# Performance work log

Measured on AMD Instinct MI355X. Metric: run time of the kernel, lower is better.

## Reference

```python
import jax, jax.numpy as jnp
import numpy as np

N_HEAD, D_MODEL, D_K, D_V, INPUT_DIM = 8, 512, 64, 64, 512
B, L = 16, 512
MASK_FILL = -1e32
LN_EPS = 1e-5


def layer_norm(x, g, b):
    m = jnp.mean(x, axis=-1, keepdims=True)
    var = jnp.mean(jnp.square(x - m), axis=-1, keepdims=True)
    return (x - m) * jax.lax.rsqrt(var + LN_EPS) * g + b


def setup_inputs() -> dict:
    key = jax.random.key(0)
    ks = jax.random.split(key, 9)
    std_qk = np.sqrt(2.0 / (D_MODEL + D_K)).astype(np.float32)
    std_v = np.sqrt(2.0 / (D_MODEL + D_V)).astype(np.float32)
    inp = {
        "q": jax.random.normal(ks[0], (B, L, INPUT_DIM), jnp.float32),
        "k": jax.random.normal(ks[1], (B, L, INPUT_DIM), jnp.float32),
        "v": jax.random.normal(ks[2], (B, L, INPUT_DIM), jnp.float32),
        # projection weights, torch Linear convention [out, in]
        "Wq": jax.random.normal(ks[3], (N_HEAD * D_K, INPUT_DIM), jnp.float32) * std_qk,
        "Wk": jax.random.normal(ks[4], (N_HEAD * D_K, INPUT_DIM), jnp.float32) * std_qk,
        "Wv": jax.random.normal(ks[5], (N_HEAD * D_V, INPUT_DIM), jnp.float32) * std_v,
        "fc1_w": jax.random.normal(ks[6], (D_MODEL, N_HEAD * D_V), jnp.float32) * 0.02,
        "fc2_w": jax.random.normal(ks[7], (D_MODEL, N_HEAD * D_V), jnp.float32) * 0.02,
        "ln1_g": jnp.ones((INPUT_DIM,), jnp.float32),
        "ln1_b": jnp.zeros((INPUT_DIM,), jnp.float32),
        "ln2_g": jnp.ones((INPUT_DIM,), jnp.float32),
        "ln2_b": jnp.zeros((INPUT_DIM,), jnp.float32),
        "ln3_g": jnp.ones((INPUT_DIM,), jnp.float32),
        "ln3_b": jnp.zeros((INPUT_DIM,), jnp.float32),
    }
    return inp


def reference(q, k, v, Wq, Wk, Wv, fc1_w, fc2_w,
              ln1_g, ln1_b, ln2_g, ln2_b, ln3_g, ln3_b):
    b, lq, _ = q.shape
    qn = layer_norm(q, ln1_g, ln1_b)
    kn = layer_norm(k, ln2_g, ln2_b)
    vn = layer_norm(v, ln3_g, ln3_b)
    # projections -> [B, L, H, d]
    qh = (qn @ Wq.T).reshape(b, lq, N_HEAD, D_K)
    kh = (kn @ Wk.T).reshape(b, lq, N_HEAD, D_K)
    vh = (vn @ Wv.T).reshape(b, lq, N_HEAD, D_V)
    # scaled dot-product attention with diagonal mask (diag_mask_flag=True)
    attn = jnp.einsum('bqhd,bkhd->bhqk', qh, kh) / jnp.sqrt(jnp.float32(D_K))
    eye = jnp.eye(lq, dtype=bool)  # diag entries masked out
    attn = jnp.where(eye[None, None], MASK_FILL, attn)
    attn = jax.nn.softmax(attn, axis=-1)
    dynamic = jnp.einsum('bhqk,bkhd->bqhd', attn, vh).reshape(b, lq, N_HEAD * D_V)
    static = vh.reshape(b, lq, N_HEAD * D_V)
    dynamic = dynamic @ fc1_w.T
    static = static @ fc2_w.T
    # attn returned in the torch layout [n_head*B, L, L] (head-major)
    attn_out = jnp.transpose(attn, (1, 0, 2, 3)).reshape(N_HEAD * b, lq, lq)
    return dynamic, static, attn_out
```

## Files before the change

kernel.cpp:

```cpp
#include <hip/hip_runtime.h>
#include <hip/hip_bf16.h>
#include <math.h>

#define NB 16
#define SEQ 512
#define DIM 512
#define NH 8
#define DHEAD 64
#define MROWS (NB*SEQ)

typedef __bf16 bf16x8 __attribute__((ext_vector_type(8)));
typedef float  f32x4  __attribute__((ext_vector_type(4)));

typedef __attribute__((address_space(1))) const unsigned int gu32c;
typedef __attribute__((address_space(3))) unsigned int lu32;

__device__ __forceinline__ void gload_lds16(const void* g, void* l) {
    __builtin_amdgcn_global_load_lds((gu32c*)g, (lu32*)l, 16, 0, 0);
}

__global__ __launch_bounds__(128)
void ln_fused_kernel(const float* __restrict__ q, const float* __restrict__ k,
                     const float* __restrict__ v,
                     const float* __restrict__ g0, const float* __restrict__ b0,
                     const float* __restrict__ g1, const float* __restrict__ b1,
                     const float* __restrict__ g2, const float* __restrict__ b2,
                     __hip_bfloat16* __restrict__ qn, __hip_bfloat16* __restrict__ kn,
                     __hip_bfloat16* __restrict__ vn) {
    const int row = blockIdx.x, which = blockIdx.y;
    const float* src = which==0 ? q : (which==1 ? k : v);
    const float* gp  = which==0 ? g0 : (which==1 ? g1 : g2);
    const float* bp  = which==0 ? b0 : (which==1 ? b1 : b2);
    __hip_bfloat16* dst = which==0 ? qn : (which==1 ? kn : vn);
    const int t = threadIdx.x;
    float4 a = *(const float4*)(src + (size_t)row*DIM + t*4);
    float s  = a.x + a.y + a.z + a.w;
    float ss = a.x*a.x + a.y*a.y + a.z*a.z + a.w*a.w;
    #pragma unroll
    for (int off = 32; off > 0; off >>= 1) {
        s  += __shfl_down(s,  off);
        ss += __shfl_down(ss, off);
    }
    __shared__ float red[4];
    if ((t & 63) == 0) { red[(t>>6)*2 + 0] = s; red[(t>>6)*2 + 1] = ss; }
    __syncthreads();
    const float S = red[0] + red[2], SS = red[1] + red[3];
    const float mean = S * (1.0f/DIM);
    const float rstd = rsqrtf(SS * (1.0f/DIM) - mean*mean + 1e-5f);
    const float4 gv = *(const float4*)(gp + t*4);
    const float4 bv = *(const float4*)(bp + t*4);
    union { ushort4 u; __hip_bfloat16 h[4]; } o;
    o.h[0] = __float2bfloat16((a.x-mean)*rstd*gv.x + bv.x);
    o.h[1] = __float2bfloat16((a.y-mean)*rstd*gv.y + bv.y);
    o.h[2] = __float2bfloat16((a.z-mean)*rstd*gv.z + bv.z);
    o.h[3] = __float2bfloat16((a.w-mean)*rstd*gv.w + bv.w);
    *(ushort4*)(dst + (size_t)row*DIM + t*4) = o.u;
}

__global__ __launch_bounds__(256)
void wconv_kernel(const float* __restrict__ w0, const float* __restrict__ w1,
                  const float* __restrict__ w2, const float* __restrict__ w3,
                  const float* __restrict__ w4, __hip_bfloat16* __restrict__ out) {
    const int m = blockIdx.y;
    const float* src = (m==0)?w0:(m==1)?w1:(m==2)?w2:(m==3)?w3:w4;
    __hip_bfloat16* dst = out + (size_t)m*DIM*DIM;
    const int i = (blockIdx.x*256 + threadIdx.x)*4;
    float4 x = *(const float4*)(src + i);
    union { ushort4 u; __hip_bfloat16 h[4]; } r;
    r.h[0]=__float2bfloat16(x.x); r.h[1]=__float2bfloat16(x.y);
    r.h[2]=__float2bfloat16(x.z); r.h[3]=__float2bfloat16(x.w);
    *(ushort4*)(dst + i) = r.u;
}

__device__ __forceinline__ void gemm_core(const __hip_bfloat16* __restrict__ A,
                                          const __hip_bfloat16* __restrict__ W,
                                          __hip_bfloat16 (&Al)[2][128*32],
                                          __hip_bfloat16 (&Bl)[2][128*32],
                                          int tid, int bm, int bn,
                                          f32x4 (&acc)[4][4]) {
    const int l = tid&63, lr = l&15, lg = l>>4;
    const int w = tid>>6, wr = w>>1, wc = w&1;
    const int grow = tid>>2, gslot = tid&3;
    const __hip_bfloat16* Ag = A + (size_t)(bm*128 + grow)*DIM + gslot*8;
    const __hip_bfloat16* Wg = W + (size_t)(bn*128 + grow)*DIM + gslot*8;

    gload_lds16(Ag,           (char*)Al[0] + tid*16);
    gload_lds16(Ag + 64*DIM,  (char*)Al[0] + 4096 + tid*16);
    gload_lds16(Wg,           (char*)Bl[0] + tid*16);
    gload_lds16(Wg + 64*DIM,  (char*)Bl[0] + 4096 + tid*16);
    __syncthreads();

    int cur = 0;
    for (int kt = 0; kt < 16; ++kt) {
        if (kt < 15) {
            const int nx = cur ^ 1;
            gload_lds16(Ag + (kt+1)*32,           (char*)Al[nx] + tid*16);
            gload_lds16(Ag + (kt+1)*32 + 64*DIM,  (char*)Al[nx] + 4096 + tid*16);
            gload_lds16(Wg + (kt+1)*32,           (char*)Bl[nx] + tid*16);
            gload_lds16(Wg + (kt+1)*32 + 64*DIM,  (char*)Bl[nx] + 4096 + tid*16);
        }
        bf16x8 af[4], bg[4];
        #pragma unroll
        for (int mi=0; mi<4; ++mi)
            af[mi] = *(const bf16x8*)((char*)Al[cur] + (wr*64 + mi*16 + lr)*64 + lg*16);
        #pragma unroll
        for (int nj=0; nj<4; ++nj)
            bg[nj] = *(const bf16x8*)((char*)Bl[cur] + (wc*64 + nj*16 + lr)*64 + lg*16);
        #pragma unroll
        for (int mi=0; mi<4; ++mi)
            #pragma unroll
            for (int nj=0; nj<4; ++nj)
                acc[mi][nj] = __builtin_amdgcn_mfma_f32_16x16x32_bf16(
                    af[mi], bg[nj], acc[mi][nj], 0, 0, 0);
        __syncthreads();
        cur ^= 1;
    }
}

__global__ __launch_bounds__(256, 3)
void gemm_qkv_kernel(const __hip_bfloat16* __restrict__ Abase,
                     const __hip_bfloat16* __restrict__ Wall,
                     __hip_bfloat16* __restrict__ qkout,
                     __hip_bfloat16* __restrict__ vhb,
                     __hip_bfloat16* __restrict__ vhT) {
    __shared__ __hip_bfloat16 Al[2][128*32];
    __shared__ __hip_bfloat16 Bl[2][128*32];
    const int tid = threadIdx.x;
    const int bm = blockIdx.x, bn = blockIdx.y, z = blockIdx.z;
    const size_t MD = (size_t)MROWS*DIM, DD = (size_t)DIM*DIM;
    const __hip_bfloat16* A = Abase + (size_t)z*MD;
    const __hip_bfloat16* W = Wall + (size_t)z*DD;
    f32x4 acc[4][4];
    #pragma unroll
    for (int mi=0; mi<4; ++mi)
        #pragma unroll
        for (int nj=0; nj<4; ++nj) acc[mi][nj] = (f32x4){0.f,0.f,0.f,0.f};
    gemm_core(A, W, Al, Bl, tid, bm, bn, acc);

    const int l = tid&63, lr = l&15, lg = l>>4;
    const int w = tid>>6, wr = w>>1, wc = w&1;
    __hip_bfloat16* dst = (z < 2) ? (qkout + (size_t)z*MD) : vhb;
    #pragma unroll
    for (int mi=0; mi<4; ++mi) {
        #pragma unroll
        for (int nj=0; nj<4; ++nj) {
            const int col = bn*128 + wc*64 + nj*16 + lr;
            const int row0 = bm*128 + wr*64 + mi*16 + lg*4;
            union { ushort4 u; __hip_bfloat16 h[4]; } pk;
            #pragma unroll
            for (int r=0; r<4; ++r) {
                const __hip_bfloat16 bv = __float2bfloat16(acc[mi][nj][r]);
                pk.h[r] = bv;
                dst[(size_t)(row0 + r)*DIM + col] = bv;
            }
            if (z == 2) {
                const int b = row0 >> 9, sp = row0 & 511;
                const int h = col >> 6, d = col & 63;
                *(ushort4*)(vhT + ((size_t)(b*NH + h)*DHEAD + d)*SEQ + sp) = pk.u;
            }
        }
    }
}

__global__ __launch_bounds__(256, 3)
void gemm_fc_kernel(const __hip_bfloat16* __restrict__ dynb,
                    const __hip_bfloat16* __restrict__ vhb,
                    const __hip_bfloat16* __restrict__ Wfc,
                    float* __restrict__ outbase) {
    __shared__ __hip_bfloat16 Al[2][128*32];
    __shared__ __hip_bfloat16 Bl[2][128*32];
    const int tid = threadIdx.x;
    const int bm = blockIdx.x, bn = blockIdx.y, z = blockIdx.z;
    const size_t MD = (size_t)MROWS*DIM, DD = (size_t)DIM*DIM;
    const __hip_bfloat16* A = z ? vhb : dynb;
    const __hip_bfloat16* W = Wfc + (size_t)z*DD;
    f32x4 acc[4][4];
    #pragma unroll
    for (int mi=0; mi<4; ++mi)
        #pragma unroll
        for (int nj=0; nj<4; ++nj) acc[mi][nj] = (f32x4){0.f,0.f,0.f,0.f};
    gemm_core(A, W, Al, Bl, tid, bm, bn, acc);

    const int l = tid&63, lr = l&15, lg = l>>4;
    const int w = tid>>6, wr = w>>1, wc = w&1;
    float* dst = outbase + (size_t)z*MD;
    #pragma unroll
    for (int mi=0; mi<4; ++mi)
        #pragma unroll
        for (int nj=0; nj<4; ++nj)
            #pragma unroll
            for (int r=0; r<4; ++r) {
                const int row = bm*128 + wr*64 + mi*16 + lg*4 + r;
                const int col = bn*128 + wc*64 + nj*16 + lr;
                dst[(size_t)row*DIM + col] = acc[mi][nj][r];
            }
}

__global__ __launch_bounds__(256)
void attn_mfma_kernel(const __hip_bfloat16* __restrict__ qhb,
                      const __hip_bfloat16* __restrict__ khb,
                      const __hip_bfloat16* __restrict__ vhT,
                      float* __restrict__ attn_out,
                      __hip_bfloat16* __restrict__ dynb) {
    __shared__ __hip_bfloat16 P_lds[16*512];
    __shared__ float redbuf[2][4][16];
    const int tid = threadIdx.x;
    const int qt = blockIdx.x, h = blockIdx.y, b = blockIdx.z;
    const int q0 = qt * 16;
    const int w  = tid >> 6;
    const int l  = tid & 63;
    const int lr = l & 15;
    const int lg = l >> 4;

    const size_t qoff = (size_t)(b*SEQ + q0 + lr)*DIM + h*DHEAD + lg*8;
    const bf16x8 qf0 = *(const bf16x8*)(qhb + qoff);
    const bf16x8 qf1 = *(const bf16x8*)(qhb + qoff + 32);

    f32x4 acc[8];
    #pragma unroll
    for (int t = 0; t < 8; ++t) acc[t] = (f32x4){0.f, 0.f, 0.f, 0.f};
    #pragma unroll
    for (int t = 0; t < 8; ++t) {
        const int kbase = w*128 + t*16;
        const size_t koff = (size_t)(b*SEQ + kbase + lr)*DIM + h*DHEAD + lg*8;
        const bf16x8 kf0 = *(const bf16x8*)(khb + koff);
        const bf16x8 kf1 = *(const bf16x8*)(khb + koff + 32);
        acc[t] = __builtin_amdgcn_mfma_f32_16x16x32_bf16(qf0, kf0, acc[t], 0, 0, 0);
        acc[t] = __builtin_amdgcn_mfma_f32_16x16x32_bf16(qf1, kf1, acc[t], 0, 0, 0);
    }

    float m[4];
    #pragma unroll
    for (int r = 0; r < 4; ++r) {
        const int grow = q0 + lg*4 + r;
        float mx = -1e30f;
        #pragma unroll
        for (int t = 0; t < 8; ++t) {
            float vv = acc[t][r] * 0.125f;
            if (w*128 + t*16 + lr == grow) vv = -1e30f;
            acc[t][r] = vv;
            mx = fmaxf(mx, vv);
        }
        #pragma unroll
        for (int off = 1; off < 16; off <<= 1) mx = fmaxf(mx, __shfl_xor(mx, off));
        m[r] = mx;
    }
    if (lr == 0) redbuf[0][w][lg*4+0] = m[0];
    if (lr == 1) redbuf[0][w][lg*4+1] = m[1];
    if (lr == 2) redbuf[0][w][lg*4+2] = m[2];
    if (lr == 3) redbuf[0][w][lg*4+3] = m[3];
    __syncthreads();
    float s[4];
    #pragma unroll
    for (int r = 0; r < 4; ++r) {
        const int rr = lg*4 + r;
        const float mx = fmaxf(fmaxf(redbuf[0][0][rr], redbuf[0][1][rr]),
                               fmaxf(redbuf[0][2][rr], redbuf[0][3][rr]));
        float sum = 0.f;
        #pragma unroll
        for (int t = 0; t < 8; ++t) {
            const float e = __expf(acc[t][r] - mx);
            acc[t][r] = e;
            sum += e;
        }
        #pragma unroll
        for (int off = 1; off < 16; off <<= 1) sum += __shfl_xor(sum, off);
        s[r] = sum;
    }
    if (lr == 0) redbuf[1][w][lg*4+0] = s[0];
    if (lr == 1) redbuf[1][w][lg*4+1] = s[1];
    if (lr == 2) redbuf[1][w][lg*4+2] = s[2];
    if (lr == 3) redbuf[1][w][lg*4+3] = s[3];
    __syncthreads();

    float* arow = attn_out + ((size_t)(h*NB + b)*SEQ + q0)*SEQ + w*128;
    #pragma unroll
    for (int r = 0; r < 4; ++r) {
        const int rr = lg*4 + r;
        const float inv = 1.0f / (redbuf[1][0][rr] + redbuf[1][1][rr] +
                                  redbuf[1][2][rr] + redbuf[1][3][rr]);
        #pragma unroll
        for (int t = 0; t < 8; ++t) {
            const float p = acc[t][r] * inv;
            arow[(size_t)rr*SEQ + t*16 + lr] = p;
            const int col = w*128 + t*16 + lr;
            int byte = rr*1024 + col*2;
            byte ^= (rr & 7) << 4;
            *(__hip_bfloat16*)((char*)P_lds + byte) = __float2bfloat16(p);
        }
    }
    __syncthreads();

    f32x4 oa = (f32x4){0.f, 0.f, 0.f, 0.f};
    f32x4 ob = (f32x4){0.f, 0.f, 0.f, 0.f};
    const size_t vbase = ((size_t)(b*NH + h)*DHEAD + w*16 + lr)*SEQ;
    #pragma unroll
    for (int ks = 0; ks < 16; ks += 2) {
        int byte0 = lr*1024 + ks*64 + lg*16;
        byte0 ^= (lr & 7) << 4;
        const bf16x8 pa0 = *(const bf16x8*)((char*)P_lds + byte0);
        const bf16x8 pb0 = *(const bf16x8*)(vhT + vbase + ks*32 + lg*8);
        oa = __builtin_amdgcn_mfma_f32_16x16x32_bf16(pa0, pb0, oa, 0, 0, 0);
        int byte1 = lr*1024 + (ks+1)*64 + lg*16;
        byte1 ^= (lr & 7) << 4;
        const bf16x8 pa1 = *(const bf16x8*)((char*)P_lds + byte1);
        const bf16x8 pb1 = *(const bf16x8*)(vhT + vbase + (ks+1)*32 + lg*8);
        ob = __builtin_amdgcn_mfma_f32_16x16x32_bf16(pa1, pb1, ob, 0, 0, 0);
    }
    #pragma unroll
    for (int r = 0; r < 4; ++r) {
        dynb[(size_t)(b*SEQ + q0 + lg*4 + r)*DIM + h*DHEAD + w*16 + lr]
            = __float2bfloat16(oa[r] + ob[r]);
    }
}

extern "C" void kernel_launch(void* const* d_in, const int* in_sizes, int n_in,
                              void* d_out, int out_size, void* d_ws, size_t ws_size,
                              hipStream_t stream) {
    const float* q    = (const float*)d_in[0];
    const float* k    = (const float*)d_in[1];
    const float* v    = (const float*)d_in[2];
    const float* Wq   = (const float*)d_in[3];
    const float* Wk   = (const float*)d_in[4];
    const float* Wv   = (const float*)d_in[5];
    const float* fc1  = (const float*)d_in[6];
    const float* fc2  = (const float*)d_in[7];
    const float* ln1g = (const float*)d_in[8];
    const float* ln1b = (const float*)d_in[9];
    const float* ln2g = (const float*)d_in[10];
    const float* ln2b = (const float*)d_in[11];
    const float* ln3g = (const float*)d_in[12];
    const float* ln3b = (const float*)d_in[13];

    const size_t DD = (size_t)DIM*DIM;
    const size_t MD = (size_t)MROWS*DIM;
    __hip_bfloat16* Wall = (__hip_bfloat16*)d_ws;
    __hip_bfloat16* qnb  = Wall + 5*DD;
    __hip_bfloat16* knb  = qnb + MD;
    __hip_bfloat16* vnb  = knb + MD;
    __hip_bfloat16* qhb  = vnb + MD;
    __hip_bfloat16* khb  = qhb + MD;
    __hip_bfloat16* vhT  = khb + MD;
    __hip_bfloat16* vhb  = vhT + MD;
    __hip_bfloat16* dynb = vhb + MD;

    float* outDyn  = (float*)d_out;
    float* outAttn = outDyn + 2*MD;

    ln_fused_kernel<<<dim3(MROWS, 3), 128, 0, stream>>>(
        q, k, v, ln1g, ln1b, ln2g, ln2b, ln3g, ln3b, qnb, knb, vnb);
    wconv_kernel<<<dim3(256, 5), 256, 0, stream>>>(Wq, Wk, Wv, fc1, fc2, Wall);

    gemm_qkv_kernel<<<dim3(MROWS/128, DIM/128, 3), 256, 0, stream>>>(
        qnb, Wall, qhb, vhb, vhT);

    attn_mfma_kernel<<<dim3(SEQ/16, NH, NB), 256, 0, stream>>>(
        qhb, khb, vhT, outAttn, dynb);

    gemm_fc_kernel<<<dim3(MROWS/128, DIM/128, 2), 256, 0, stream>>>(
        dynb, vhb, Wall + 3*DD, outDyn);
}
```

Measured before the change: 324.1 us.

## Swizzle GEMM LDS tiles and deepen async prefetch with explicit waitcnt barriers

Applies an XOR swizzle to the 16-byte slot index on both the global-to-LDS writes and the LDS fragment reads, to reduce bank conflicts. Restructures the double-buffered k-loop so two stages are in flight at once, using explicit vmcnt waits and raw s_barrier instead of __syncthreads. The aim is to overlap global loads with MFMA work more fully. In exchange it relies on hand-written waitcnt counts and scheduling barriers being correct, which adds a risk of subtle races.

```diff
diff --git a/kernel.cpp b/kernel.cpp
--- a/kernel.cpp
+++ b/kernel.cpp
@@ -80,41 +80,53 @@
                                           f32x4 (&acc)[4][4]) {
     const int l = tid&63, lr = l&15, lg = l>>4;
     const int w = tid>>6, wr = w>>1, wc = w&1;
-    const int grow = tid>>2, gslot = tid&3;
-    const __hip_bfloat16* Ag = A + (size_t)(bm*128 + grow)*DIM + gslot*8;
-    const __hip_bfloat16* Wg = W + (size_t)(bn*128 + grow)*DIM + gslot*8;
-
-    gload_lds16(Ag,           (char*)Al[0] + tid*16);
-    gload_lds16(Ag + 64*DIM,  (char*)Al[0] + 4096 + tid*16);
-    gload_lds16(Wg,           (char*)Bl[0] + tid*16);
-    gload_lds16(Wg + 64*DIM,  (char*)Bl[0] + 4096 + tid*16);
-    __syncthreads();
-
-    int cur = 0;
-    for (int kt = 0; kt < 16; ++kt) {
-        if (kt < 15) {
-            const int nx = cur ^ 1;
-            gload_lds16(Ag + (kt+1)*32,           (char*)Al[nx] + tid*16);
-            gload_lds16(Ag + (kt+1)*32 + 64*DIM,  (char*)Al[nx] + 4096 + tid*16);
-            gload_lds16(Wg + (kt+1)*32,           (char*)Bl[nx] + tid*16);
-            gload_lds16(Wg + (kt+1)*32 + 64*DIM,  (char*)Bl[nx] + 4096 + tid*16);
-        }
+    const int row0  = tid >> 2;
+    const int gslot = (tid&3) ^ ((row0>>1)&3);
+    const __hip_bfloat16* Ag = A + (size_t)(bm*128 + row0)*DIM + gslot*8;
+    const __hip_bfloat16* Wg = W + (size_t)(bn*128 + row0)*DIM + gslot*8;
+    const int tsw = (lg ^ ((lr>>1)&3)) << 4;
+
+    auto STAGE = [&](int kt, int buf) {
+        gload_lds16(Ag + kt*32,           (char*)Al[buf] + tid*16);
+        gload_lds16(Ag + kt*32 + 64*DIM,  (char*)Al[buf] + 4096 + tid*16);
+        gload_lds16(Wg + kt*32,           (char*)Bl[buf] + tid*16);
+        gload_lds16(Wg + kt*32 + 64*DIM,  (char*)Bl[buf] + 4096 + tid*16);
+    };
+    auto COMPUTE = [&](int buf) {
         bf16x8 af[4], bg[4];
         #pragma unroll
         for (int mi=0; mi<4; ++mi)
-            af[mi] = *(const bf16x8*)((char*)Al[cur] + (wr*64 + mi*16 + lr)*64 + lg*16);
+            af[mi] = *(const bf16x8*)((char*)Al[buf] + (wr*64 + mi*16 + lr)*64 + tsw);
         #pragma unroll
         for (int nj=0; nj<4; ++nj)
-            bg[nj] = *(const bf16x8*)((char*)Bl[cur] + (wc*64 + nj*16 + lr)*64 + lg*16);
+            bg[nj] = *(const bf16x8*)((char*)Bl[buf] + (wc*64 + nj*16 + lr)*64 + tsw);
+        asm volatile("s_waitcnt lgkmcnt(0)" ::: "memory");
+        __builtin_amdgcn_sched_barrier(0);
         #pragma unroll
         for (int mi=0; mi<4; ++mi)
             #pragma unroll
             for (int nj=0; nj<4; ++nj)
                 acc[mi][nj] = __builtin_amdgcn_mfma_f32_16x16x32_bf16(
                     af[mi], bg[nj], acc[mi][nj], 0, 0, 0);
-        __syncthreads();
+    };
+
+    STAGE(0, 0);
+    STAGE(1, 1);
+    int cur = 0;
+    for (int kt = 0; kt < 15; ++kt) {
+        asm volatile("s_waitcnt vmcnt(4)" ::: "memory");
+        __builtin_amdgcn_s_barrier();
+        __builtin_amdgcn_sched_barrier(0);
+        COMPUTE(cur);
+        __builtin_amdgcn_s_barrier();
+        __builtin_amdgcn_sched_barrier(0);
+        if (kt < 14) STAGE(kt+2, cur);
         cur ^= 1;
     }
+    asm volatile("s_waitcnt vmcnt(0)" ::: "memory");
+    __builtin_amdgcn_s_barrier();
+    __builtin_amdgcn_sched_barrier(0);
+    COMPUTE(cur);
 }
 
 __global__ __launch_bounds__(256, 3)
```

Measured after the change: 326.4 us. About the same (+0.7%).

## Replace double-buffered GEMM core with full-K weight strip in LDS, A from global

Applied to the files above, without the earlier changes.

The projection and FC GEMMs switch from a 128x128 tile with double-buffered A/B K-slices to a 128x64 tile. The block loads the whole 64x512 weight strip into XOR-swizzled LDS once, and each wave streams its A fragments straight from global memory. This removes the per-K-step barriers and A staging through LDS. In exchange it uses 64KB of LDS per block, lowers occupancy to 2 blocks, doubles the grid and halves per-wave MFMA reuse, so A reads rely on cache.

```diff
diff --git a/kernel.cpp b/kernel.cpp
--- a/kernel.cpp
+++ b/kernel.cpp
@@ -72,80 +72,73 @@
     *(ushort4*)(dst + i) = r.u;
 }
 
-__device__ __forceinline__ void gemm_core(const __hip_bfloat16* __restrict__ A,
-                                          const __hip_bfloat16* __restrict__ W,
-                                          __hip_bfloat16 (&Al)[2][128*32],
-                                          __hip_bfloat16 (&Bl)[2][128*32],
-                                          int tid, int bm, int bn,
-                                          f32x4 (&acc)[4][4]) {
-    const int l = tid&63, lr = l&15, lg = l>>4;
-    const int w = tid>>6, wr = w>>1, wc = w&1;
-    const int grow = tid>>2, gslot = tid&3;
-    const __hip_bfloat16* Ag = A + (size_t)(bm*128 + grow)*DIM + gslot*8;
-    const __hip_bfloat16* Wg = W + (size_t)(bn*128 + grow)*DIM + gslot*8;
-
-    gload_lds16(Ag,           (char*)Al[0] + tid*16);
-    gload_lds16(Ag + 64*DIM,  (char*)Al[0] + 4096 + tid*16);
-    gload_lds16(Wg,           (char*)Bl[0] + tid*16);
-    gload_lds16(Wg + 64*DIM,  (char*)Bl[0] + 4096 + tid*16);
-    __syncthreads();
-
-    int cur = 0;
-    for (int kt = 0; kt < 16; ++kt) {
-        if (kt < 15) {
-            const int nx = cur ^ 1;
-            gload_lds16(Ag + (kt+1)*32,           (char*)Al[nx] + tid*16);
-            gload_lds16(Ag + (kt+1)*32 + 64*DIM,  (char*)Al[nx] + 4096 + tid*16);
-            gload_lds16(Wg + (kt+1)*32,           (char*)Bl[nx] + tid*16);
-            gload_lds16(Wg + (kt+1)*32 + 64*DIM,  (char*)Bl[nx] + 4096 + tid*16);
-        }
-        bf16x8 af[4], bg[4];
-        #pragma unroll
-        for (int mi=0; mi<4; ++mi)
-            af[mi] = *(const bf16x8*)((char*)Al[cur] + (wr*64 + mi*16 + lr)*64 + lg*16);
-        #pragma unroll
-        for (int nj=0; nj<4; ++nj)
-            bg[nj] = *(const bf16x8*)((char*)Bl[cur] + (wc*64 + nj*16 + lr)*64 + lg*16);
-        #pragma unroll
-        for (int mi=0; mi<4; ++mi)
-            #pragma unroll
-            for (int nj=0; nj<4; ++nj)
-                acc[mi][nj] = __builtin_amdgcn_mfma_f32_16x16x32_bf16(
-                    af[mi], bg[nj], acc[mi][nj], 0, 0, 0);
-        __syncthreads();
-        cur ^= 1;
-    }
-}
-
-__global__ __launch_bounds__(256, 3)
+__device__ __forceinline__ void strip_core(const __hip_bfloat16* __restrict__ A,
+                                           const __hip_bfloat16* __restrict__ W,
+                                           __hip_bfloat16* Wl,
+                                           int tid, int bm, int bn,
+                                           f32x4 (&acc)[2][4]) {
+    {
+        const int sub = tid >> 6;
+        const int t64 = tid & 63;
+        #pragma unroll
+        for (int i = 0; i < 16; ++i) {
+            const int row = i*4 + sub;
+            const int inrow = (t64*16) ^ ((row & 7) << 4);
+            gload_lds16((const char*)(W + (size_t)(bn*64 + row)*DIM) + inrow,
+                        (char*)Wl + i*4096 + tid*16);
+        }
+    }
+    __syncthreads();
+
+    const int l = tid & 63, lr = l & 15, lg = l >> 4;
+    const int w = tid >> 6;
+    const int m0 = bm*128 + w*32;
+    const __hip_bfloat16* Ar0 = A + (size_t)(m0 + lr)*DIM + lg*8;
+    const __hip_bfloat16* Ar1 = A + (size_t)(m0 + 16 + lr)*DIM + lg*8;
+
+    #pragma unroll
+    for (int kk = 0; kk < 16; ++kk) {
+        const bf16x8 a0 = *(const bf16x8*)(Ar0 + kk*32);
+        const bf16x8 a1 = *(const bf16x8*)(Ar1 + kk*32);
+        #pragma unroll
+        for (int nj = 0; nj < 4; ++nj) {
+            const int row = nj*16 + lr;
+            const int byte = row*1024 + ((kk*64 + lg*16) ^ ((row & 7) << 4));
+            const bf16x8 bgf = *(const bf16x8*)((char*)Wl + byte);
+            acc[0][nj] = __builtin_amdgcn_mfma_f32_16x16x32_bf16(a0, bgf, acc[0][nj], 0, 0, 0);
+            acc[1][nj] = __builtin_amdgcn_mfma_f32_16x16x32_bf16(a1, bgf, acc[1][nj], 0, 0, 0);
+        }
+    }
+}
+
+__global__ __launch_bounds__(256, 2)
 void gemm_qkv_kernel(const __hip_bfloat16* __restrict__ Abase,
                      const __hip_bfloat16* __restrict__ Wall,
                      __hip_bfloat16* __restrict__ qkout,
                      __hip_bfloat16* __restrict__ vhb,
                      __hip_bfloat16* __restrict__ vhT) {
-    __shared__ __hip_bfloat16 Al[2][128*32];
-    __shared__ __hip_bfloat16 Bl[2][128*32];
+    __shared__ __hip_bfloat16 Wl[64*512];
     const int tid = threadIdx.x;
     const int bm = blockIdx.x, bn = blockIdx.y, z = blockIdx.z;
     const size_t MD = (size_t)MROWS*DIM, DD = (size_t)DIM*DIM;
     const __hip_bfloat16* A = Abase + (size_t)z*MD;
     const __hip_bfloat16* W = Wall + (size_t)z*DD;
-    f32x4 acc[4][4];
-    #pragma unroll
-    for (int mi=0; mi<4; ++mi)
+    f32x4 acc[2][4];
+    #pragma unroll
+    for (int mi=0; mi<2; ++mi)
         #pragma unroll
         for (int nj=0; nj<4; ++nj) acc[mi][nj] = (f32x4){0.f,0.f,0.f,0.f};
-    gemm_core(A, W, Al, Bl, tid, bm, bn, acc);
+    strip_core(A, W, Wl, tid, bm, bn, acc);
 
     const int l = tid&63, lr = l&15, lg = l>>4;
-    const int w = tid>>6, wr = w>>1, wc = w&1;
+    const int w = tid>>6;
     __hip_bfloat16* dst = (z < 2) ? (qkout + (size_t)z*MD) : vhb;
     #pragma unroll
-    for (int mi=0; mi<4; ++mi) {
+    for (int mi=0; mi<2; ++mi) {
         #pragma unroll
         for (int nj=0; nj<4; ++nj) {
-            const int col = bn*128 + wc*64 + nj*16 + lr;
-            const int row0 = bm*128 + wr*64 + mi*16 + lg*4;
+            const int col = bn*64 + nj*16 + lr;
+            const int row0 = bm*128 + w*32 + mi*16 + lg*4;
             union { ushort4 u; __hip_bfloat16 h[4]; } pk;
             #pragma unroll
             for (int r=0; r<4; ++r) {
@@ -162,36 +155,35 @@
     }
 }
 
-__global__ __launch_bounds__(256, 3)
+__global__ __launch_bounds__(256, 2)
 void gemm_fc_kernel(const __hip_bfloat16* __restrict__ dynb,
                     const __hip_bfloat16* __restrict__ vhb,
                     const __hip_bfloat16* __restrict__ Wfc,
                     float* __restrict__ outbase) {
-    __shared__ __hip_bfloat16 Al[2][128*32];
-    __shared__ __hip_bfloat16 Bl[2][128*32];
+    __shared__ __hip_bfloat16 Wl[64*512];
     const int tid = threadIdx.x;
     const int bm = blockIdx.x, bn = blockIdx.y, z = blockIdx.z;
     const size_t MD = (size_t)MROWS*DIM, DD = (size_t)DIM*DIM;
     const __hip_bfloat16* A = z ? vhb : dynb;
     const __hip_bfloat16* W = Wfc + (size_t)z*DD;
-    f32x4 acc[4][4];
-    #pragma unroll
-    for (int mi=0; mi<4; ++mi)
+    f32x4 acc[2][4];
+    #pragma unroll
+    for (int mi=0; mi<2; ++mi)
         #pragma unroll
         for (int nj=0; nj<4; ++nj) acc[mi][nj] = (f32x4){0.f,0.f,0.f,0.f};
-    gemm_core(A, W, Al, Bl, tid, bm, bn, acc);
+    strip_core(A, W, Wl, tid, bm, bn, acc);
 
     const int l = tid&63, lr = l&15, lg = l>>4;
-    const int w = tid>>6, wr = w>>1, wc = w&1;
+    const int w = tid>>6;
     float* dst = outbase + (size_t)z*MD;
     #pragma unroll
-    for (int mi=0; mi<4; ++mi)
+    for (int mi=0; mi<2; ++mi)
         #pragma unroll
         for (int nj=0; nj<4; ++nj)
             #pragma unroll
             for (int r=0; r<4; ++r) {
-                const int row = bm*128 + wr*64 + mi*16 + lg*4 + r;
-                const int col = bn*128 + wc*64 + nj*16 + lr;
+                const int row = bm*128 + w*32 + mi*16 + lg*4 + r;
+                const int col = bn*64 + nj*16 + lr;
                 dst[(size_t)row*DIM + col] = acc[mi][nj][r];
             }
 }
@@ -351,12 +343,12 @@
         q, k, v, ln1g, ln1b, ln2g, ln2b, ln3g, ln3b, qnb, knb, vnb);
     wconv_kernel<<<dim3(256, 5), 256, 0, stream>>>(Wq, Wk, Wv, fc1, fc2, Wall);
 
-    gemm_qkv_kernel<<<dim3(MROWS/128, DIM/128, 3), 256, 0, stream>>>(
+    gemm_qkv_kernel<<<dim3(MROWS/128, DIM/64, 3), 256, 0, stream>>>(
         qnb, Wall, qhb, vhb, vhT);
 
     attn_mfma_kernel<<<dim3(SEQ/16, NH, NB), 256, 0, stream>>>(
         qhb, khb, vhT, outAttn, dynb);
 
-    gemm_fc_kernel<<<dim3(MROWS/128, DIM/128, 2), 256, 0, stream>>>(
+    gemm_fc_kernel<<<dim3(MROWS/128, DIM/64, 2), 256, 0, stream>>>(
         dynb, vhb, Wall + 3*DD, outDyn);
 }
```

New measurement: 344.5 us. 1.06x slower.
